# Kernel optimization log

Measured on AMD Instinct MI355X. Metric: run time of the kernel, lower is better.

The kernel has to match this reference:

```python
import jax, jax.numpy as jnp
import numpy as np

D_MODEL = 1024
N_HEADS = 16
D_HEAD = 64


def setup_inputs() -> dict:
    key = jax.random.key(0)
    kx, kq, kk, kv, ko = jax.random.split(key, 5)
    B, T = 2, 2048
    inner = N_HEADS * D_HEAD
    s = 1.0 / np.sqrt(D_MODEL)
    return {
        "x": jax.random.normal(kx, (B, T, D_MODEL), dtype=jnp.float32),
        "Wq": jax.random.normal(kq, (D_MODEL, inner), dtype=jnp.float32) * s,
        "Wk": jax.random.normal(kk, (D_MODEL, inner), dtype=jnp.float32) * s,
        "Wv": jax.random.normal(kv, (D_MODEL, inner), dtype=jnp.float32) * s,
        "Wo": jax.random.normal(ko, (inner, D_MODEL), dtype=jnp.float32) * (1.0 / np.sqrt(inner)),
    }


def reference(x, Wq, Wk, Wv, Wo):
    B, T, D = x.shape
    H, d = N_HEADS, D_HEAD
    q = (x @ Wq).reshape(B, T, H, d)
    k = (x @ Wk).reshape(B, T, H, d)
    v = (x @ Wv).reshape(B, T, H, d)
    # scale=False -> no 1/sqrt(d) scaling
    scores = jnp.einsum('bthd,bshd->bhts', q, k)
    # strictly-lower-triangular mask (tril with diagonal=-1): s < t kept
    mask = jnp.tril(jnp.ones((T, T), dtype=bool), k=-1)
    scores = jnp.where(mask, scores, 0.0)
    out = jnp.einsum('bhts,bshd->bthd', scores, v).reshape(B, T, H * d)
    return out @ Wo
```

## Files before the change

kernel.cpp:

```cpp
#include <hip/hip_runtime.h>
#include <hip/hip_bf16.h>

#define TSEQ   2048
#define DM     1024
#define NHEAD  16
#define DH     64
#define BATCH  2
#define MR     (BATCH * TSEQ)
#define CH     64
#define NC     (TSEQ / CH)
#define QKVLD  (3 * DM)
#define LP     72

typedef __attribute__((ext_vector_type(8))) short bf16x8;
typedef __attribute__((ext_vector_type(4))) float f32x4;

__device__ __forceinline__ short f2bf(float x) {
  __hip_bfloat16 h = __float2bfloat16(x);
  return *reinterpret_cast<short*>(&h);
}

__device__ __forceinline__ void stage16(const void* g, void* l) {
  __builtin_amdgcn_global_load_lds(
      (const __attribute__((address_space(1))) void*)g,
      (__attribute__((address_space(3))) void*)l, 16, 0, 0);
}

__device__ __forceinline__ void store_elem(float v, float* p) { *p = v; }
__device__ __forceinline__ void store_elem(float v, __hip_bfloat16* p) { *p = __float2bfloat16(v); }

template <typename OutT, int TN>
__global__ __launch_bounds__(256) void gemm_bf16(const short* __restrict__ A,
                                                 const short* __restrict__ Bt,
                                                 OutT* __restrict__ C,
                                                 int M, int N, int K, int ldc) {
  constexpr int NF = TN / 32;
  __shared__ short As[128][32];
  __shared__ short Bs[TN][32];
  const int tid = threadIdx.x;
  const int lane = tid & 63, wid = tid >> 6;
  const int wave_m = wid >> 1, wave_n = wid & 1;

  const unsigned nwg = gridDim.x * gridDim.y;
  const unsigned lin = blockIdx.y * gridDim.x + blockIdx.x;
  const unsigned q8 = nwg >> 3, r8 = nwg & 7;
  const unsigned xcd = lin & 7, idx = lin >> 3;
  const unsigned swz = (xcd < r8 ? xcd * (q8 + 1) : r8 * (q8 + 1) + (xcd - r8) * q8) + idx;
  const int bx = swz % gridDim.x, by = swz / gridDim.x;

  const int row0 = by * 128, col0 = bx * TN;

  const int sr = tid >> 2, sk = (tid & 3) * 8;
  const short* Ag0 = A + (size_t)(row0 + sr) * K + sk;
  const short* Bg0 = Bt + (size_t)(col0 + sr) * K + sk;
  short* AsL = &As[0][0] + tid * 8;
  short* BsL = &Bs[0][0] + tid * 8;

  f32x4 acc[4][NF];
#pragma unroll
  for (int i = 0; i < 4; ++i)
#pragma unroll
    for (int j = 0; j < NF; ++j) acc[i][j] = (f32x4){0.f, 0.f, 0.f, 0.f};

  const int fm = wave_m * 64 + (lane & 15);
  const int fn = wave_n * (TN / 2) + (lane & 15);
  const int fk = (lane >> 4) * 8;

  for (int k0 = 0; k0 < K; k0 += 32) {
    stage16(Ag0 + k0, AsL);
    stage16(Ag0 + (size_t)64 * K + k0, AsL + 2048);
    stage16(Bg0 + k0, BsL);
    if constexpr (TN == 128) stage16(Bg0 + (size_t)64 * K + k0, BsL + 2048);
    __syncthreads();
    bf16x8 af[4], bf[NF];
#pragma unroll
    for (int t = 0; t < 4; ++t) af[t] = *(const bf16x8*)&As[fm + t * 16][fk];
#pragma unroll
    for (int t = 0; t < NF; ++t) bf[t] = *(const bf16x8*)&Bs[fn + t * 16][fk];
#pragma unroll
    for (int im = 0; im < 4; ++im)
#pragma unroll
      for (int jn = 0; jn < NF; ++jn)
        acc[im][jn] = __builtin_amdgcn_mfma_f32_16x16x32_bf16(af[im], bf[jn], acc[im][jn], 0, 0, 0);
    __syncthreads();
  }

  const int crow = (lane >> 4) * 4, ccol = lane & 15;
#pragma unroll
  for (int im = 0; im < 4; ++im)
#pragma unroll
    for (int jn = 0; jn < NF; ++jn) {
      OutT* Cp = C + (size_t)(row0 + wave_m * 64 + im * 16 + crow) * ldc
                   + col0 + wave_n * (TN / 2) + jn * 16 + ccol;
#pragma unroll
      for (int r = 0; r < 4; ++r) store_elem(acc[im][jn][r], Cp + (size_t)r * ldc);
    }
}

__global__ __launch_bounds__(256) void cvt_bf16(const float* __restrict__ in,
                                                __hip_bfloat16* __restrict__ out, int n) {
  int i = (blockIdx.x * 256 + threadIdx.x) * 4;
  if (i >= n) return;
  float4 v = *(const float4*)(in + i);
  union { __hip_bfloat16 h[4]; uint2 u; } pk;
  pk.h[0] = __float2bfloat16(v.x); pk.h[1] = __float2bfloat16(v.y);
  pk.h[2] = __float2bfloat16(v.z); pk.h[3] = __float2bfloat16(v.w);
  *(uint2*)(out + i) = pk.u;
}

__global__ __launch_bounds__(256) void transposeW4(const float* __restrict__ W0,
                                                   const float* __restrict__ W1,
                                                   const float* __restrict__ W2,
                                                   const float* __restrict__ W3,
                                                   __hip_bfloat16* __restrict__ Wt) {
  const float* W = blockIdx.z == 0 ? W0 : blockIdx.z == 1 ? W1 : blockIdx.z == 2 ? W2 : W3;
  __hip_bfloat16* out = Wt + (size_t)blockIdx.z * DM * DM;
  __shared__ float tile[64][65];
  const int tid = threadIdx.x;
  const int kt = blockIdx.y * 64, nt = blockIdx.x * 64;
  const int lr = tid >> 6, lc = tid & 63;
#pragma unroll
  for (int i = 0; i < 16; ++i) {
    int k = i * 4 + lr;
    tile[k][lc] = W[(size_t)(kt + k) * DM + nt + lc];
  }
  __syncthreads();
  const int nl = tid >> 4, k4 = (tid & 15) * 4;
#pragma unroll
  for (int i = 0; i < 4; ++i) {
    int n = i * 16 + nl;
    union { __hip_bfloat16 h[4]; uint2 u; } pk;
#pragma unroll
    for (int x = 0; x < 4; ++x) pk.h[x] = __float2bfloat16(tile[k4 + x][n]);
    *(uint2*)(out + (size_t)(nt + n) * DM + kt + k4) = pk.u;
  }
}

__global__ __launch_bounds__(256) void chunk_kv(const __hip_bfloat16* __restrict__ QKV,
                                                float* __restrict__ Mc) {
  const int c = blockIdx.x, h = blockIdx.y, b = blockIdx.z;
  __shared__ short Kt[DH][LP];
  __shared__ short Vt[DH][LP];
  const int tid = threadIdx.x;
  const int lane = tid & 63, w = tid >> 6;
  const int r = tid >> 2, q16 = (tid & 3) * 16;
  const short* qkv = (const short*)QKV;
  const size_t grow = ((size_t)(b * TSEQ + c * CH + r)) * QKVLD + h * DH;
  short kk[16], vv[16];
  *(bf16x8*)&kk[0] = *(const bf16x8*)(qkv + grow + DM + q16);
  *(bf16x8*)&kk[8] = *(const bf16x8*)(qkv + grow + DM + q16 + 8);
  *(bf16x8*)&vv[0] = *(const bf16x8*)(qkv + grow + 2 * DM + q16);
  *(bf16x8*)&vv[8] = *(const bf16x8*)(qkv + grow + 2 * DM + q16 + 8);
#pragma unroll
  for (int j = 0; j < 16; ++j) {
    Kt[q16 + j][r] = kk[j];
    Vt[q16 + j][r] = vv[j];
  }
  __syncthreads();

  const int m = lane & 15, q = lane >> 4;
  bf16x8 af[2];
  af[0] = *(const bf16x8*)&Vt[16 * w + m][q * 8];
  af[1] = *(const bf16x8*)&Vt[16 * w + m][q * 8 + 32];
  f32x4 acc[4];
#pragma unroll
  for (int ct = 0; ct < 4; ++ct) acc[ct] = (f32x4){0.f, 0.f, 0.f, 0.f};
#pragma unroll
  for (int ct = 0; ct < 4; ++ct) {
    bf16x8 b0 = *(const bf16x8*)&Kt[ct * 16 + m][q * 8];
    bf16x8 b1 = *(const bf16x8*)&Kt[ct * 16 + m][q * 8 + 32];
    acc[ct] = __builtin_amdgcn_mfma_f32_16x16x32_bf16(af[0], b0, acc[ct], 0, 0, 0);
    acc[ct] = __builtin_amdgcn_mfma_f32_16x16x32_bf16(af[1], b1, acc[ct], 0, 0, 0);
  }
  float* out = Mc + ((size_t)((b * NHEAD + h) * NC + c)) * (DH * DH);
#pragma unroll
  for (int ct = 0; ct < 4; ++ct)
#pragma unroll
    for (int rr = 0; rr < 4; ++rr) {
      int row = 16 * w + q * 4 + rr, col = ct * 16 + m;
      out[(size_t)row * DH + col] = acc[ct][rr];
    }
}

__global__ __launch_bounds__(256) void scan_states(const float* __restrict__ Mc,
                                                   __hip_bfloat16* __restrict__ Spre) {
  const int bh = blockIdx.y;
  const size_t off = (size_t)bh * NC * (DH * DH) + blockIdx.x * 256 + threadIdx.x;
  const float* src = Mc + off;
  __hip_bfloat16* dst = Spre + off;
  float run = 0.f;
  for (int c = 0; c < NC; ++c) {
    dst[(size_t)c * (DH * DH)] = __float2bfloat16(run);
    run += src[(size_t)c * (DH * DH)];
  }
}

__global__ __launch_bounds__(256) void intra_attn(const __hip_bfloat16* __restrict__ QKV,
                                                  const __hip_bfloat16* __restrict__ Spre,
                                                  __hip_bfloat16* __restrict__ O_) {
  const int c = blockIdx.x, h = blockIdx.y, b = blockIdx.z;
  __shared__ short Qs[CH][LP];
  __shared__ short Ks[CH][LP];
  __shared__ short Vt[DH][LP];
  __shared__ short St[DH][LP];
  const int tid = threadIdx.x;
  const int lane = tid & 63, w = tid >> 6;
  const int r = tid >> 2, q16 = (tid & 3) * 16;
  const short* qkv = (const short*)QKV;
  const size_t grow = ((size_t)(b * TSEQ + c * CH + r)) * QKVLD + h * DH;
  *(bf16x8*)&Qs[r][q16]     = *(const bf16x8*)(qkv + grow + q16);
  *(bf16x8*)&Qs[r][q16 + 8] = *(const bf16x8*)(qkv + grow + q16 + 8);
  *(bf16x8*)&Ks[r][q16]     = *(const bf16x8*)(qkv + grow + DM + q16);
  *(bf16x8*)&Ks[r][q16 + 8] = *(const bf16x8*)(qkv + grow + DM + q16 + 8);
  const short* Sg = (const short*)Spre + ((size_t)((b * NHEAD + h) * NC + c)) * (DH * DH);
  *(bf16x8*)&St[r][q16]     = *(const bf16x8*)(Sg + r * DH + q16);
  *(bf16x8*)&St[r][q16 + 8] = *(const bf16x8*)(Sg + r * DH + q16 + 8);
  short vv[16];
  *(bf16x8*)&vv[0] = *(const bf16x8*)(qkv + grow + 2 * DM + q16);
  *(bf16x8*)&vv[8] = *(const bf16x8*)(qkv + grow + 2 * DM + q16 + 8);
#pragma unroll
  for (int j = 0; j < 16; ++j) Vt[q16 + j][r] = vv[j];
  __syncthreads();

  const int m = lane & 15, q = lane >> 4;
  bf16x8 af[2];
  af[0] = *(const bf16x8*)&Qs[16 * w + m][q * 8];
  af[1] = *(const bf16x8*)&Qs[16 * w + m][q * 8 + 32];
  f32x4 acc[4], pacc[4];
#pragma unroll
  for (int ct = 0; ct < 4; ++ct) {
    acc[ct] = (f32x4){0.f, 0.f, 0.f, 0.f};
    pacc[ct] = (f32x4){0.f, 0.f, 0.f, 0.f};
  }
#pragma unroll
  for (int ct = 0; ct < 4; ++ct) {
    bf16x8 s0 = *(const bf16x8*)&St[ct * 16 + m][q * 8];
    bf16x8 s1 = *(const bf16x8*)&St[ct * 16 + m][q * 8 + 32];
    acc[ct] = __builtin_amdgcn_mfma_f32_16x16x32_bf16(af[0], s0, acc[ct], 0, 0, 0);
    acc[ct] = __builtin_amdgcn_mfma_f32_16x16x32_bf16(af[1], s1, acc[ct], 0, 0, 0);
    bf16x8 k0 = *(const bf16x8*)&Ks[ct * 16 + m][q * 8];
    bf16x8 k1 = *(const bf16x8*)&Ks[ct * 16 + m][q * 8 + 32];
    pacc[ct] = __builtin_amdgcn_mfma_f32_16x16x32_bf16(af[0], k0, pacc[ct], 0, 0, 0);
    pacc[ct] = __builtin_amdgcn_mfma_f32_16x16x32_bf16(af[1], k1, pacc[ct], 0, 0, 0);
  }
  __syncthreads();
#pragma unroll
  for (int ct = 0; ct < 4; ++ct) {
    int col = ct * 16 + m;
#pragma unroll
    for (int rr = 0; rr < 4; ++rr) {
      int row = 16 * w + q * 4 + rr;
      float pv = (col < row) ? pacc[ct][rr] : 0.f;
      Qs[row][col] = f2bf(pv);
    }
  }
  __syncthreads();
  bf16x8 pf[2];
  pf[0] = *(const bf16x8*)&Qs[16 * w + m][q * 8];
  pf[1] = *(const bf16x8*)&Qs[16 * w + m][q * 8 + 32];
#pragma unroll
  for (int ct = 0; ct < 4; ++ct) {
    bf16x8 v0 = *(const bf16x8*)&Vt[ct * 16 + m][q * 8];
    bf16x8 v1 = *(const bf16x8*)&Vt[ct * 16 + m][q * 8 + 32];
    acc[ct] = __builtin_amdgcn_mfma_f32_16x16x32_bf16(pf[0], v0, acc[ct], 0, 0, 0);
    acc[ct] = __builtin_amdgcn_mfma_f32_16x16x32_bf16(pf[1], v1, acc[ct], 0, 0, 0);
  }
  __hip_bfloat16* Ob = O_ + ((size_t)(b * TSEQ + c * CH)) * DM + h * DH;
#pragma unroll
  for (int ct = 0; ct < 4; ++ct)
#pragma unroll
    for (int rr = 0; rr < 4; ++rr) {
      int row = 16 * w + q * 4 + rr, col = ct * 16 + m;
      Ob[(size_t)row * DM + col] = __float2bfloat16(acc[ct][rr]);
    }
}

extern "C" void kernel_launch(void* const* d_in, const int* in_sizes, int n_in,
                              void* d_out, int out_size, void* d_ws, size_t ws_size,
                              hipStream_t stream) {
  const float* x  = (const float*)d_in[0];
  const float* Wq = (const float*)d_in[1];
  const float* Wk = (const float*)d_in[2];
  const float* Wv = (const float*)d_in[3];
  const float* Wo = (const float*)d_in[4];
  float* out = (float*)d_out;

  char* ws = (char*)d_ws;
  __hip_bfloat16* xb    = (__hip_bfloat16*)ws;  ws += (size_t)MR * DM * 2;
  __hip_bfloat16* WtAll = (__hip_bfloat16*)ws;  ws += (size_t)4 * DM * DM * 2;
  __hip_bfloat16* qkvb  = (__hip_bfloat16*)ws;  ws += (size_t)MR * QKVLD * 2;
  float*          Mc    = (float*)ws;           ws += (size_t)BATCH * NHEAD * NC * DH * DH * 4;
  __hip_bfloat16* Spre  = (__hip_bfloat16*)ws;  ws += (size_t)BATCH * NHEAD * NC * DH * DH * 2;
  __hip_bfloat16* aob   = (__hip_bfloat16*)ws;  ws += (size_t)MR * DM * 2;

  cvt_bf16<<<(MR * DM / 4 + 255) / 256, 256, 0, stream>>>(x, xb, MR * DM);
  transposeW4<<<dim3(DM / 64, DM / 64, 4), 256, 0, stream>>>(Wq, Wk, Wv, Wo, WtAll);

  gemm_bf16<__hip_bfloat16, 128><<<dim3(QKVLD / 128, MR / 128), 256, 0, stream>>>(
      (const short*)xb, (const short*)WtAll, qkvb, MR, QKVLD, DM, QKVLD);

  chunk_kv<<<dim3(NC, NHEAD, BATCH), 256, 0, stream>>>(qkvb, Mc);
  scan_states<<<dim3(DH * DH / 256, BATCH * NHEAD), 256, 0, stream>>>(Mc, Spre);
  intra_attn<<<dim3(NC, NHEAD, BATCH), 256, 0, stream>>>(qkvb, Spre, aob);

  gemm_bf16<float, 64><<<dim3(DM / 64, MR / 128), 256, 0, stream>>>(
      (const short*)aob, (const short*)(WtAll + (size_t)3 * DM * DM), out, MR, DM, DM, DM);
}
```

Measured before the change: 167.2 us.

## Double GEMM K-tile to 64 with XOR-swizzled LDS and fuse prep kernels

The bf16 GEMM now stages a 64-wide K slice per iteration instead of 32, which halves the number of barrier pairs per K loop. The LDS layout is XOR-swizzled by row so fragment reads avoid bank conflicts. The fp32-to-bf16 conversion of x and the four weight transposes are merged into a single launch, saving one kernel launch. In exchange the GEMM uses twice the LDS per block, which may lower occupancy, and the conversion blocks in the merged kernel use a grid-stride loop.

```diff
diff --git a/kernel.cpp b/kernel.cpp
--- a/kernel.cpp
+++ b/kernel.cpp
@@ -35,8 +35,9 @@
                                                  OutT* __restrict__ C,
                                                  int M, int N, int K, int ldc) {
   constexpr int NF = TN / 32;
-  __shared__ short As[128][32];
-  __shared__ short Bs[TN][32];
+  constexpr int BSW = TN / 32;
+  __shared__ short As[128][64];
+  __shared__ short Bs[TN][64];
   const int tid = threadIdx.x;
   const int lane = tid & 63, wid = tid >> 6;
   const int wave_m = wid >> 1, wave_n = wid & 1;
@@ -50,9 +51,10 @@
 
   const int row0 = by * 128, col0 = bx * TN;
 
-  const int sr = tid >> 2, sk = (tid & 3) * 8;
-  const short* Ag0 = A + (size_t)(row0 + sr) * K + sk;
-  const short* Bg0 = Bt + (size_t)(col0 + sr) * K + sk;
+  const int sr = tid >> 3;
+  const int scs = ((tid & 7) ^ (sr & 7)) * 8;
+  const short* Ag0 = A + (size_t)(row0 + sr) * K + scs;
+  const short* Bg0 = Bt + (size_t)(col0 + sr) * K + scs;
   short* AsL = &As[0][0] + tid * 8;
   short* BsL = &Bs[0][0] + tid * 8;
 
@@ -62,26 +64,38 @@
 #pragma unroll
     for (int j = 0; j < NF; ++j) acc[i][j] = (f32x4){0.f, 0.f, 0.f, 0.f};
 
-  const int fm = wave_m * 64 + (lane & 15);
-  const int fn = wave_n * (TN / 2) + (lane & 15);
+  const int frow_a = wave_m * 64 + (lane & 15);
+  const int frow_b = wave_n * (TN / 2) + (lane & 15);
   const int fk = (lane >> 4) * 8;
-
-  for (int k0 = 0; k0 < K; k0 += 32) {
-    stage16(Ag0 + k0, AsL);
-    stage16(Ag0 + (size_t)64 * K + k0, AsL + 2048);
-    stage16(Bg0 + k0, BsL);
-    if constexpr (TN == 128) stage16(Bg0 + (size_t)64 * K + k0, BsL + 2048);
+  const int rx = (lane & 7) << 4;
+
+  for (int k0 = 0; k0 < K; k0 += 64) {
+#pragma unroll
+    for (int j = 0; j < 4; ++j)
+      stage16(Ag0 + (size_t)(j * 32) * K + k0, AsL + j * 2048);
+#pragma unroll
+    for (int j = 0; j < BSW; ++j)
+      stage16(Bg0 + (size_t)(j * 32) * K + k0, BsL + j * 2048);
     __syncthreads();
-    bf16x8 af[4], bf[NF];
-#pragma unroll
-    for (int t = 0; t < 4; ++t) af[t] = *(const bf16x8*)&As[fm + t * 16][fk];
-#pragma unroll
-    for (int t = 0; t < NF; ++t) bf[t] = *(const bf16x8*)&Bs[fn + t * 16][fk];
-#pragma unroll
-    for (int im = 0; im < 4; ++im)
-#pragma unroll
-      for (int jn = 0; jn < NF; ++jn)
-        acc[im][jn] = __builtin_amdgcn_mfma_f32_16x16x32_bf16(af[im], bf[jn], acc[im][jn], 0, 0, 0);
+#pragma unroll
+    for (int kk = 0; kk < 64; kk += 32) {
+      bf16x8 af[4], bfr[NF];
+#pragma unroll
+      for (int t = 0; t < 4; ++t) {
+        int R = frow_a + t * 16;
+        af[t] = *(const bf16x8*)((const char*)&As[0][0] + R * 128 + ((((kk + fk) * 2)) ^ rx));
+      }
+#pragma unroll
+      for (int t = 0; t < NF; ++t) {
+        int R = frow_b + t * 16;
+        bfr[t] = *(const bf16x8*)((const char*)&Bs[0][0] + R * 128 + ((((kk + fk) * 2)) ^ rx));
+      }
+#pragma unroll
+      for (int im = 0; im < 4; ++im)
+#pragma unroll
+        for (int jn = 0; jn < NF; ++jn)
+          acc[im][jn] = __builtin_amdgcn_mfma_f32_16x16x32_bf16(af[im], bfr[jn], acc[im][jn], 0, 0, 0);
+    }
     __syncthreads();
   }
 
@@ -97,25 +111,28 @@
     }
 }
 
-__global__ __launch_bounds__(256) void cvt_bf16(const float* __restrict__ in,
-                                                __hip_bfloat16* __restrict__ out, int n) {
-  int i = (blockIdx.x * 256 + threadIdx.x) * 4;
-  if (i >= n) return;
-  float4 v = *(const float4*)(in + i);
-  union { __hip_bfloat16 h[4]; uint2 u; } pk;
-  pk.h[0] = __float2bfloat16(v.x); pk.h[1] = __float2bfloat16(v.y);
-  pk.h[2] = __float2bfloat16(v.z); pk.h[3] = __float2bfloat16(v.w);
-  *(uint2*)(out + i) = pk.u;
-}
-
-__global__ __launch_bounds__(256) void transposeW4(const float* __restrict__ W0,
-                                                   const float* __restrict__ W1,
-                                                   const float* __restrict__ W2,
-                                                   const float* __restrict__ W3,
-                                                   __hip_bfloat16* __restrict__ Wt) {
+__global__ __launch_bounds__(256) void prep(const float* __restrict__ x,
+                                            const float* __restrict__ W0,
+                                            const float* __restrict__ W1,
+                                            const float* __restrict__ W2,
+                                            const float* __restrict__ W3,
+                                            __hip_bfloat16* __restrict__ xb,
+                                            __hip_bfloat16* __restrict__ Wt) {
+  __shared__ float tile[64][65];
+  if (blockIdx.z == 4) {
+    int i = ((blockIdx.y * gridDim.x + blockIdx.x) * 256 + threadIdx.x) * 4;
+    const int stride = 16 * 16 * 256 * 4;
+    for (; i < MR * DM; i += stride) {
+      float4 v = *(const float4*)(x + i);
+      union { __hip_bfloat16 h[4]; uint2 u; } pk;
+      pk.h[0] = __float2bfloat16(v.x); pk.h[1] = __float2bfloat16(v.y);
+      pk.h[2] = __float2bfloat16(v.z); pk.h[3] = __float2bfloat16(v.w);
+      *(uint2*)(xb + i) = pk.u;
+    }
+    return;
+  }
   const float* W = blockIdx.z == 0 ? W0 : blockIdx.z == 1 ? W1 : blockIdx.z == 2 ? W2 : W3;
   __hip_bfloat16* out = Wt + (size_t)blockIdx.z * DM * DM;
-  __shared__ float tile[64][65];
   const int tid = threadIdx.x;
   const int kt = blockIdx.y * 64, nt = blockIdx.x * 64;
   const int lr = tid >> 6, lc = tid & 63;
@@ -131,7 +148,7 @@
     int n = i * 16 + nl;
     union { __hip_bfloat16 h[4]; uint2 u; } pk;
 #pragma unroll
-    for (int x = 0; x < 4; ++x) pk.h[x] = __float2bfloat16(tile[k4 + x][n]);
+    for (int xx = 0; xx < 4; ++xx) pk.h[xx] = __float2bfloat16(tile[k4 + xx][n]);
     *(uint2*)(out + (size_t)(nt + n) * DM + kt + k4) = pk.u;
   }
 }
@@ -293,8 +310,7 @@
   __hip_bfloat16* Spre  = (__hip_bfloat16*)ws;  ws += (size_t)BATCH * NHEAD * NC * DH * DH * 2;
   __hip_bfloat16* aob   = (__hip_bfloat16*)ws;  ws += (size_t)MR * DM * 2;
 
-  cvt_bf16<<<(MR * DM / 4 + 255) / 256, 256, 0, stream>>>(x, xb, MR * DM);
-  transposeW4<<<dim3(DM / 64, DM / 64, 4), 256, 0, stream>>>(Wq, Wk, Wv, Wo, WtAll);
+  prep<<<dim3(16, 16, 5), 256, 0, stream>>>(x, Wq, Wk, Wv, Wo, xb, WtAll);
 
   gemm_bf16<__hip_bfloat16, 128><<<dim3(QKVLD / 128, MR / 128), 256, 0, stream>>>(
       (const short*)xb, (const short*)WtAll, qkvb, MR, QKVLD, DM, QKVLD);
```

After: 157.7 us. -5.7%, faster.
